# Optimization experiments

Hardware: AMD Instinct MI355X
Metric: run time of the kernel (lower is better)

Reference implementation:

```python
import jax, jax.numpy as jnp
import numpy as np
from math import ceil

EMBED = 512
HEADS = 8
HD = EMBED // HEADS  # 64
FFN = 2048
MIN_CHUNK = 32
LN_EPS = 1e-5


def layer_norm(x, g, b):
    mu = jnp.mean(x, axis=-1, keepdims=True)
    var = jnp.var(x, axis=-1, keepdims=True)
    return (x - mu) * jax.lax.rsqrt(var + LN_EPS) * g + b


def masked_attention(q, k, v, mask_bool, L):
    # q,k,v: [B*H, L, HD]; mask_bool: [B*H, L] (True = padding)
    BH = q.shape[0]
    S = max(MIN_CHUNK, ceil(L / 4))  # dynamic chunk size (static given L)
    C = ceil(L / S)
    pad = C * S - L
    if pad:
        q = jnp.pad(q, ((0, 0), (0, pad), (0, 0)))
        k = jnp.pad(k, ((0, 0), (0, pad), (0, 0)))
        v = jnp.pad(v, ((0, 0), (0, pad), (0, 0)))
        mask_bool = jnp.pad(mask_bool, ((0, 0), (0, pad)), constant_values=True)
    qc = q.reshape(BH, C, S, HD)
    kc = k.reshape(BH, C, S, HD)
    vc = v.reshape(BH, C, S, HD)
    mc = mask_bool.reshape(BH, C, S)
    # pad one phantom (fully masked) chunk on each side, then gather 3-chunk windows
    kp = jnp.pad(kc, ((0, 0), (1, 1), (0, 0), (0, 0)))
    vp = jnp.pad(vc, ((0, 0), (1, 1), (0, 0), (0, 0)))
    mp = jnp.pad(mc, ((0, 0), (1, 1), (0, 0)), constant_values=True)
    k_win = jnp.concatenate([kp[:, i:i + C] for i in range(3)], axis=2)  # [BH,C,3S,HD]
    v_win = jnp.concatenate([vp[:, i:i + C] for i in range(3)], axis=2)
    m_win = jnp.concatenate([mp[:, i:i + C] for i in range(3)], axis=2)  # [BH,C,3S]
    scores = jnp.einsum('bcqd,bckd->bcqk', qc, k_win) / jnp.sqrt(jnp.float32(HD))
    scores = jnp.where(m_win[:, :, None, :], -jnp.inf, scores)
    w = jax.nn.softmax(scores, axis=-1)
    out = jnp.einsum('bcqk,bckd->bcqd', w, v_win)
    return out.reshape(BH, C * S, HD)[:, :L]


def setup_inputs() -> dict:
    key = jax.random.key(0)
    ks = jax.random.split(key, 6)
    B, L, D = 4, 2048, EMBED
    s = 0.02
    return {
        'x': jax.random.normal(ks[0], (B, L, D), jnp.float32),
        'mask': jnp.zeros((B, L), jnp.int32),
        'qkv_w': jax.random.normal(ks[1], (D, 3 * D), jnp.float32) * s,
        'qkv_b': jnp.zeros((3 * D,), jnp.float32),
        'out_w': jax.random.normal(ks[2], (D, D), jnp.float32) * s,
        'out_b': jnp.zeros((D,), jnp.float32),
        'ffn_w1': jax.random.normal(ks[3], (D, FFN), jnp.float32) * s,
        'ffn_b1': jnp.zeros((FFN,), jnp.float32),
        'ffn_w2': jax.random.normal(ks[4], (FFN, D), jnp.float32) * s,
        'ffn_b2': jnp.zeros((D,), jnp.float32),
        'ln1_g': jnp.ones((D,), jnp.float32),
        'ln1_b': jnp.zeros((D,), jnp.float32),
        'ln2_g': jnp.ones((D,), jnp.float32),
        'ln2_b': jnp.zeros((D,), jnp.float32),
    }


def reference(x, mask, qkv_w, qkv_b, out_w, out_b, ffn_w1, ffn_b1, ffn_w2, ffn_b2, ln1_g, ln1_b, ln2_g, ln2_b):
    B, L, D = x.shape
    qkv = x @ qkv_w + qkv_b
    q, k, v = jnp.split(qkv, 3, axis=-1)

    def to_heads(t):
        return t.reshape(B, L, HEADS, HD).transpose(0, 2, 1, 3).reshape(B * HEADS, L, HD)

    mb = jnp.broadcast_to(mask.astype(bool)[:, None, :], (B, HEADS, L)).reshape(B * HEADS, L)
    a = masked_attention(to_heads(q), to_heads(k), to_heads(v), mb, L)
    a = a.reshape(B, HEADS, L, HD).transpose(0, 2, 1, 3).reshape(B, L, D)
    x = x + (a @ out_w + out_b)  # dropout is identity in eval
    x = layer_norm(x, ln1_g, ln1_b)
    h = jax.nn.gelu(x @ ffn_w1 + ffn_b1, approximate=False) @ ffn_w2 + ffn_b2
    x = layer_norm(x + h, ln2_g, ln2_b)
    return x
```

## Files before the change

### kernel.cpp

```cpp
#include <hip/hip_runtime.h>
#include <hip/hip_bf16.h>
#include <math.h>

#define EMBED 512
#define HEADS 8
#define HD    64
#define FFN_  2048
#define NB    4
#define LSEQ  2048
#define MROWS (NB*LSEQ)
#define BHN   (NB*HEADS)

typedef __attribute__((ext_vector_type(8))) short bf16x8;
typedef __attribute__((ext_vector_type(4))) float f32x4;
#define MFMA16(a,b,c) __builtin_amdgcn_mfma_f32_16x16x32_bf16(a,b,c,0,0,0)

__device__ __forceinline__ unsigned short f2bf(float f) {
    unsigned int u = __float_as_uint(f);
    u += 0x7fff + ((u >> 16) & 1);
    return (unsigned short)(u >> 16);
}
__device__ __forceinline__ float bf2f(unsigned short u) {
    return __uint_as_float(((unsigned int)u) << 16);
}
__device__ __forceinline__ unsigned int cvt_pk_bf16(float lo, float hi) {
    unsigned int r;
    asm("v_cvt_pk_bf16_f32 %0, %1, %2" : "=v"(r) : "v"(lo), "v"(hi));
    return r;
}
__device__ __forceinline__ void gl_lds16(const unsigned short* g, unsigned short* l) {
    __builtin_amdgcn_global_load_lds(
        (const __attribute__((address_space(1))) unsigned int*)g,
        (__attribute__((address_space(3))) unsigned int*)l, 16, 0, 0);
}
__device__ __forceinline__ float gelu_f(float x) {
    float u = x * fmaf(x * x, 0.044715f, 1.0f) * 0.7978845608f;
    float a = fminf(fmaxf(u * 2.885390082f, -30.f), 30.f);
    float t = __builtin_amdgcn_exp2f(a);
    return x * t * __builtin_amdgcn_rcpf(t + 1.0f);
}
__device__ __forceinline__ void xcd_swz(int& bx, int& by, int gx, int gy) {
    int nwg = gx * gy;
    int lid = by * gx + bx;
    int cpx = nwg >> 3;
    int swz = (lid & 7) * cpx + (lid >> 3);
    bx = swz % gx;
    by = swz / gx;
}


__global__ __launch_bounds__(256) void cvt_bf16(const float* __restrict__ in,
                                                unsigned short* __restrict__ out, int n) {
    int i = (blockIdx.x * 256 + threadIdx.x) * 8;
    if (i >= n) return;
    float4 a = *reinterpret_cast<const float4*>(&in[i]);
    float4 b = *reinterpret_cast<const float4*>(&in[i + 4]);
    unsigned short t[8] = {f2bf(a.x), f2bf(a.y), f2bf(a.z), f2bf(a.w),
                           f2bf(b.x), f2bf(b.y), f2bf(b.z), f2bf(b.w)};
    *reinterpret_cast<uint4*>(&out[i]) = *reinterpret_cast<uint4*>(t);
}

__global__ __launch_bounds__(256) void wtrans(const float* __restrict__ in,
                                              unsigned short* __restrict__ out,
                                              int K, int N) {
    __shared__ float tile[32][33];
    const int k0 = blockIdx.y * 32, n0 = blockIdx.x * 32;
    const int t = threadIdx.x;
    const int r = t >> 3, c = (t & 7) * 4;
    float4 v = *reinterpret_cast<const float4*>(&in[(size_t)(k0 + r) * N + n0 + c]);
    tile[r][c] = v.x; tile[r][c + 1] = v.y; tile[r][c + 2] = v.z; tile[r][c + 3] = v.w;
    __syncthreads();
    unsigned short tmp[4] = {f2bf(tile[c + 0][r]), f2bf(tile[c + 1][r]),
                             f2bf(tile[c + 2][r]), f2bf(tile[c + 3][r])};
    *reinterpret_cast<uint2*>(&out[(size_t)(n0 + r) * K + k0 + c]) =
        *reinterpret_cast<uint2*>(tmp);
}

__global__ __launch_bounds__(256) void vtransp(const unsigned short* __restrict__ v,
                                               unsigned short* __restrict__ vT) {
    __shared__ unsigned short tile[64][72];
    const int bh = blockIdx.y, l0 = blockIdx.x * 64;
    const int t = threadIdx.x;
    #pragma unroll
    for (int u = 0; u < 2; ++u) {
        int id = t + u * 256; int r = id >> 3, c = (id & 7) * 8;
        *reinterpret_cast<uint4*>(&tile[r][c]) = *reinterpret_cast<const uint4*>(
            &v[((size_t)bh * LSEQ + l0 + r) * HD + c]);
    }
    __syncthreads();
    #pragma unroll
    for (int u = 0; u < 2; ++u) {
        int id = t + u * 256; int d = id >> 3, kc = (id & 7) * 8;
        unsigned short tmp[8];
        #pragma unroll
        for (int jj = 0; jj < 8; ++jj) {
            int kap = kc + jj;
            tmp[jj] = tile[(kap & 3) * 16 + (kap >> 2)][d];
        }
        *reinterpret_cast<uint4*>(&vT[((size_t)bh * HD + d) * LSEQ + l0 + kc]) =
            *reinterpret_cast<uint4*>(tmp);
    }
}

template<int MODE>
__global__ __launch_bounds__(256) void gemm_bf16(
    const unsigned short* __restrict__ A, const unsigned short* __restrict__ WT,
    const float* __restrict__ bias,
    void* __restrict__ o0, void* __restrict__ o1, void* __restrict__ o2,
    int M, int N, int K)
{
    __shared__ unsigned short As[128 * 64];
    __shared__ unsigned short Bs[128 * 64];
    int bx = blockIdx.x, by = blockIdx.y;
    xcd_swz(bx, by, gridDim.x, gridDim.y);
    const int t = threadIdx.x;
    const int m0 = by * 128, n0 = bx * 128;
    const int w = t >> 6, lane = t & 63;
    const int wm = (w >> 1) * 64, wn = (w & 1) * 64;
    const int lr = lane & 15, lk = (lane >> 4) * 8;
    const int rb = (lane >> 4) * 4;
    const int srow = lane >> 3, scol = (lane & 7) * 8;

    f32x4 zero = {0.f, 0.f, 0.f, 0.f};
    f32x4 acc[4][4];
    #pragma unroll
    for (int i = 0; i < 4; ++i)
        #pragma unroll
        for (int j = 0; j < 4; ++j) acc[i][j] = zero;

    for (int k0 = 0; k0 < K; k0 += 64) {
        __syncthreads();
        #pragma unroll
        for (int i = 0; i < 4; ++i) {
            const int seg = w * 4 + i;
            const int r = seg * 8 + srow;
            gl_lds16(A  + (size_t)(m0 + r) * K + k0 + scol, &As[seg * 512 + lane * 8]);
            gl_lds16(WT + (size_t)(n0 + r) * K + k0 + scol, &Bs[seg * 512 + lane * 8]);
        }
        __syncthreads();
        #pragma unroll
        for (int kk = 0; kk < 2; ++kk) {
            bf16x8 a[4], b[4];
            #pragma unroll
            for (int i = 0; i < 4; ++i)
                a[i] = *reinterpret_cast<const bf16x8*>(&As[(wm + i * 16 + lr) * 64 + kk * 32 + lk]);
            #pragma unroll
            for (int j = 0; j < 4; ++j)
                b[j] = *reinterpret_cast<const bf16x8*>(&Bs[(wn + j * 16 + lr) * 64 + kk * 32 + lk]);
            #pragma unroll
            for (int i = 0; i < 4; ++i)
                #pragma unroll
                for (int j = 0; j < 4; ++j)
                    acc[i][j] = MFMA16(a[i], b[j], acc[i][j]);
        }
    }

    #pragma unroll
    for (int i = 0; i < 4; ++i) {
        #pragma unroll
        for (int j = 0; j < 4; ++j) {
            const int n = n0 + wn + j * 16 + lr;
            const float bv = bias[n];
            #pragma unroll
            for (int r = 0; r < 4; ++r) {
                const int m = m0 + wm + i * 16 + rb + r;
                float val = acc[i][j][r] + bv;
                if (MODE == 0) {
                    const int which = n >> 9, nn = n & 511, hs = nn >> 6, d = nn & 63;
                    const int bh = (m >> 11) * 8 + hs, l = m & 2047;
                    unsigned short* p = (which == 0) ? (unsigned short*)o0
                                      : (which == 1) ? (unsigned short*)o1
                                                     : (unsigned short*)o2;
                    p[((size_t)bh * LSEQ + l) * HD + d] = f2bf(val);
                } else {
                    size_t idx = (size_t)m * N + n;
                    ((unsigned short*)o0)[idx] = f2bf(gelu_f(val));
                }
            }
        }
    }
}

template<int MODE>
__global__ __launch_bounds__(256) void gemm64(
    const unsigned short* __restrict__ A, const unsigned short* __restrict__ WT,
    const float* __restrict__ bias, const void* __restrict__ res,
    void* __restrict__ out, int M, int N, int K)
{
    __shared__ unsigned short As[64 * 64];
    __shared__ unsigned short Bs[64 * 64];
    int bx = blockIdx.x, by = blockIdx.y;
    xcd_swz(bx, by, gridDim.x, gridDim.y);
    const int t = threadIdx.x;
    const int m0 = by * 64, n0 = bx * 64;
    const int w = t >> 6, lane = t & 63;
    const int wm = (w >> 1) * 32, wn = (w & 1) * 32;
    const int lr = lane & 15, lk = (lane >> 4) * 8;
    const int rb = (lane >> 4) * 4;
    const int srow = t >> 3, scol = (t & 7) * 8;

    f32x4 zero = {0.f, 0.f, 0.f, 0.f};
    f32x4 acc[2][2];
    #pragma unroll
    for (int i = 0; i < 2; ++i)
        #pragma unroll
        for (int j = 0; j < 2; ++j) acc[i][j] = zero;

    for (int k0 = 0; k0 < K; k0 += 64) {
        __syncthreads();
        gl_lds16(A  + (size_t)(m0 + srow)      * K + k0 + scol, &As[t * 8]);
        gl_lds16(A  + (size_t)(m0 + 32 + srow) * K + k0 + scol, &As[2048 + t * 8]);
        gl_lds16(WT + (size_t)(n0 + srow)      * K + k0 + scol, &Bs[t * 8]);
        gl_lds16(WT + (size_t)(n0 + 32 + srow) * K + k0 + scol, &Bs[2048 + t * 8]);
        __syncthreads();
        #pragma unroll
        for (int kk = 0; kk < 2; ++kk) {
            bf16x8 a[2], b[2];
            #pragma unroll
            for (int i = 0; i < 2; ++i)
                a[i] = *reinterpret_cast<const bf16x8*>(&As[(wm + i * 16 + lr) * 64 + kk * 32 + lk]);
            #pragma unroll
            for (int j = 0; j < 2; ++j)
                b[j] = *reinterpret_cast<const bf16x8*>(&Bs[(wn + j * 16 + lr) * 64 + kk * 32 + lk]);
            #pragma unroll
            for (int i = 0; i < 2; ++i)
                #pragma unroll
                for (int j = 0; j < 2; ++j)
                    acc[i][j] = MFMA16(a[i], b[j], acc[i][j]);
        }
    }

    #pragma unroll
    for (int i = 0; i < 2; ++i) {
        #pragma unroll
        for (int j = 0; j < 2; ++j) {
            const int n = n0 + wn + j * 16 + lr;
            const float bv = bias[n];
            #pragma unroll
            for (int r = 0; r < 4; ++r) {
                const int m = m0 + wm + i * 16 + rb + r;
                size_t idx = (size_t)m * N + n;
                float val = acc[i][j][r] + bv;
                if (MODE == 0) {
                    val += ((const float*)res)[idx];
                    ((unsigned short*)out)[idx] = f2bf(val);
                } else {
                    val += bf2f(((const unsigned short*)res)[idx]);
                    ((float*)out)[idx] = val;
                }
            }
        }
    }
}

__global__ __launch_bounds__(256) void attn_mfma(
    const unsigned short* __restrict__ Q, const unsigned short* __restrict__ K,
    const unsigned short* __restrict__ VTp, const int* __restrict__ mask,
    unsigned short* __restrict__ out)
{
    __shared__ unsigned short Ks[64][72];
    __shared__ unsigned short Vs[64][72];
    __shared__ unsigned short Ps[128][72];
    __shared__ float kbl[64];

    int bx = blockIdx.x, by = blockIdx.y;
    xcd_swz(bx, by, 16, 32);
    const int qt = bx, bh = by;
    const int b = bh >> 3, hh = bh & 7;
    const int t = threadIdx.x, w = t >> 6, lane = t & 63;
    const int lr = lane & 15, hi = lane >> 4;
    const int lk = hi * 8, rb = hi * 4;
    const int qr0 = qt * 128;
    const int c = qr0 >> 9;
    const int kstart = max(0, (c - 1) * 512), kend = min(LSEQ, (c + 2) * 512);

    const float C1  = 0.18033688f;
    const float KB0 = -14.4269504f;

    bf16x8 qf[2][2];
    #pragma unroll
    for (int fi = 0; fi < 2; ++fi)
        #pragma unroll
        for (int kk = 0; kk < 2; ++kk)
            qf[fi][kk] = *reinterpret_cast<const bf16x8*>(
                &Q[((size_t)bh * LSEQ + qr0 + w * 32 + fi * 16 + lr) * HD + kk * 32 + lk]);

    f32x4 zero = {0.f, 0.f, 0.f, 0.f};
    f32x4 acc[2][4];
    float lsum[2][4];
    #pragma unroll
    for (int fi = 0; fi < 2; ++fi) {
        #pragma unroll
        for (int j = 0; j < 4; ++j) acc[fi][j] = zero;
        #pragma unroll
        for (int r = 0; r < 4; ++r) lsum[fi][r] = 0.f;
    }

    for (int kg = kstart; kg < kend; kg += 64) {
        __syncthreads();
        #pragma unroll
        for (int u = 0; u < 2; ++u) {
            int id = t + u * 256; int r = id >> 3, kc = (id & 7) * 8;
            *reinterpret_cast<uint4*>(&Ks[r][kc]) = *reinterpret_cast<const uint4*>(
                &K[((size_t)bh * LSEQ + kg + r) * HD + kc]);
            *reinterpret_cast<uint4*>(&Vs[r][kc]) = *reinterpret_cast<const uint4*>(
                &VTp[((size_t)bh * HD + r) * LSEQ + kg + kc]);
        }
        if (t < 64) kbl[t] = mask[b * LSEQ + kg + t] ? -1e30f : KB0;
        __syncthreads();

        f32x4 s[2][4];
        #pragma unroll
        for (int fi = 0; fi < 2; ++fi)
            #pragma unroll
            for (int j = 0; j < 4; ++j) s[fi][j] = zero;
        #pragma unroll
        for (int kk = 0; kk < 2; ++kk) {
            #pragma unroll
            for (int j = 0; j < 4; ++j) {
                bf16x8 bk = *reinterpret_cast<const bf16x8*>(&Ks[j * 16 + lr][kk * 32 + lk]);
                s[0][j] = MFMA16(qf[0][kk], bk, s[0][j]);
                s[1][j] = MFMA16(qf[1][kk], bk, s[1][j]);
            }
        }
        #pragma unroll
        for (int fi = 0; fi < 2; ++fi) {
            #pragma unroll
            for (int r = 0; r < 4; ++r) {
                float p0 = __builtin_amdgcn_exp2f(fmaf(s[fi][0][r], C1, kbl[0 * 16 + lr]));
                float p1 = __builtin_amdgcn_exp2f(fmaf(s[fi][1][r], C1, kbl[1 * 16 + lr]));
                float p2 = __builtin_amdgcn_exp2f(fmaf(s[fi][2][r], C1, kbl[2 * 16 + lr]));
                float p3 = __builtin_amdgcn_exp2f(fmaf(s[fi][3][r], C1, kbl[3 * 16 + lr]));
                lsum[fi][r] += (p0 + p1) + (p2 + p3);
                uint2 pw;
                pw.x = cvt_pk_bf16(p0, p1);
                pw.y = cvt_pk_bf16(p2, p3);
                *reinterpret_cast<uint2*>(&Ps[w * 32 + fi * 16 + rb + r][lr * 4]) = pw;
            }
        }
        #pragma unroll
        for (int kk = 0; kk < 2; ++kk) {
            bf16x8 pa0 = *reinterpret_cast<const bf16x8*>(&Ps[w * 32 + lr][kk * 32 + lk]);
            bf16x8 pa1 = *reinterpret_cast<const bf16x8*>(&Ps[w * 32 + 16 + lr][kk * 32 + lk]);
            #pragma unroll
            for (int j = 0; j < 4; ++j) {
                bf16x8 bv = *reinterpret_cast<const bf16x8*>(&Vs[j * 16 + lr][kk * 32 + lk]);
                acc[0][j] = MFMA16(pa0, bv, acc[0][j]);
                acc[1][j] = MFMA16(pa1, bv, acc[1][j]);
            }
        }
    }

    float linv[2][4];
    #pragma unroll
    for (int fi = 0; fi < 2; ++fi)
        #pragma unroll
        for (int r = 0; r < 4; ++r) {
            float v = lsum[fi][r];
            v += __shfl_xor(v, 1, 16);
            v += __shfl_xor(v, 2, 16);
            v += __shfl_xor(v, 4, 16);
            v += __shfl_xor(v, 8, 16);
            linv[fi][r] = 1.0f / v;
        }
    #pragma unroll
    for (int fi = 0; fi < 2; ++fi)
        #pragma unroll
        for (int j = 0; j < 4; ++j)
            #pragma unroll
            for (int r = 0; r < 4; ++r) {
                const int l = qr0 + w * 32 + fi * 16 + rb + r;
                const int d = j * 16 + lr;
                out[((size_t)(b * LSEQ + l)) * EMBED + hh * HD + d] =
                    f2bf(acc[fi][j][r] * linv[fi][r]);
            }
}

__global__ __launch_bounds__(256) void ln_b2b(
    const unsigned short* __restrict__ in, const float* __restrict__ g,
    const float* __restrict__ bt, unsigned short* __restrict__ out)
{
    const int t = threadIdx.x, lane = t & 63;
    const int row = blockIdx.x * 4 + (t >> 6);
    uint4 raw = *reinterpret_cast<const uint4*>(&in[(size_t)row * EMBED + lane * 8]);
    float v[8];
    const unsigned int* rw = reinterpret_cast<const unsigned int*>(&raw);
    #pragma unroll
    for (int i = 0; i < 4; ++i) {
        v[2 * i]     = __uint_as_float(rw[i] << 16);
        v[2 * i + 1] = __uint_as_float(rw[i] & 0xffff0000u);
    }
    float s = 0.f, ss = 0.f;
    #pragma unroll
    for (int i = 0; i < 8; ++i) { s += v[i]; ss += v[i] * v[i]; }
    #pragma unroll
    for (int off = 1; off < 64; off <<= 1) {
        s  += __shfl_xor(s, off);
        ss += __shfl_xor(ss, off);
    }
    const float mu = s * (1.0f / EMBED);
    const float var = ss * (1.0f / EMBED) - mu * mu;
    const float rs = rsqrtf(var + 1e-5f);
    float4 g0 = *reinterpret_cast<const float4*>(&g[lane * 8]);
    float4 g1 = *reinterpret_cast<const float4*>(&g[lane * 8 + 4]);
    float4 b0 = *reinterpret_cast<const float4*>(&bt[lane * 8]);
    float4 b1 = *reinterpret_cast<const float4*>(&bt[lane * 8 + 4]);
    float gg[8] = {g0.x, g0.y, g0.z, g0.w, g1.x, g1.y, g1.z, g1.w};
    float bb[8] = {b0.x, b0.y, b0.z, b0.w, b1.x, b1.y, b1.z, b1.w};
    unsigned short o[8];
    #pragma unroll
    for (int i = 0; i < 8; ++i) o[i] = f2bf((v[i] - mu) * rs * gg[i] + bb[i]);
    *reinterpret_cast<uint4*>(&out[(size_t)row * EMBED + lane * 8]) =
        *reinterpret_cast<uint4*>(o);
}

__global__ __launch_bounds__(256) void ln_f2f(
    const float* __restrict__ in, const float* __restrict__ g,
    const float* __restrict__ bt, float* __restrict__ out)
{
    const int t = threadIdx.x, lane = t & 63;
    const int row = blockIdx.x * 4 + (t >> 6);
    const float* x = in + (size_t)row * EMBED + lane * 8;
    float4 a = *reinterpret_cast<const float4*>(x);
    float4 b2 = *reinterpret_cast<const float4*>(x + 4);
    float v[8] = {a.x, a.y, a.z, a.w, b2.x, b2.y, b2.z, b2.w};
    float s = 0.f, ss = 0.f;
    #pragma unroll
    for (int i = 0; i < 8; ++i) { s += v[i]; ss += v[i] * v[i]; }
    #pragma unroll
    for (int off = 1; off < 64; off <<= 1) {
        s  += __shfl_xor(s, off);
        ss += __shfl_xor(ss, off);
    }
    const float mu = s * (1.0f / EMBED);
    const float var = ss * (1.0f / EMBED) - mu * mu;
    const float rs = rsqrtf(var + 1e-5f);
    float4 g0 = *reinterpret_cast<const float4*>(&g[lane * 8]);
    float4 g1 = *reinterpret_cast<const float4*>(&g[lane * 8 + 4]);
    float4 b0 = *reinterpret_cast<const float4*>(&bt[lane * 8]);
    float4 b1 = *reinterpret_cast<const float4*>(&bt[lane * 8 + 4]);
    float gg[8] = {g0.x, g0.y, g0.z, g0.w, g1.x, g1.y, g1.z, g1.w};
    float bb[8] = {b0.x, b0.y, b0.z, b0.w, b1.x, b1.y, b1.z, b1.w};
    float o[8];
    #pragma unroll
    for (int i = 0; i < 8; ++i) o[i] = (v[i] - mu) * rs * gg[i] + bb[i];
    float* op = out + (size_t)row * EMBED + lane * 8;
    *reinterpret_cast<float4*>(op)     = make_float4(o[0], o[1], o[2], o[3]);
    *reinterpret_cast<float4*>(op + 4) = make_float4(o[4], o[5], o[6], o[7]);
}

extern "C" void kernel_launch(void* const* d_in, const int* in_sizes, int n_in,
                              void* d_out, int out_size, void* d_ws, size_t ws_size,
                              hipStream_t stream) {
    const float* x      = (const float*)d_in[0];
    const int*   mask   = (const int*)  d_in[1];
    const float* qkv_w  = (const float*)d_in[2];
    const float* qkv_b  = (const float*)d_in[3];
    const float* out_w  = (const float*)d_in[4];
    const float* out_b  = (const float*)d_in[5];
    const float* ffn_w1 = (const float*)d_in[6];
    const float* ffn_b1 = (const float*)d_in[7];
    const float* ffn_w2 = (const float*)d_in[8];
    const float* ffn_b2 = (const float*)d_in[9];
    const float* ln1_g  = (const float*)d_in[10];
    const float* ln1_b  = (const float*)d_in[11];
    const float* ln2_g  = (const float*)d_in[12];
    const float* ln2_b  = (const float*)d_in[13];

    char* wsb = (char*)d_ws;
    unsigned short* qkv_wT = (unsigned short*)(wsb + 0);
    unsigned short* out_wT = (unsigned short*)(wsb + 1572864);
    unsigned short* w1T    = (unsigned short*)(wsb + 2097152);
    unsigned short* w2T    = (unsigned short*)(wsb + 4194304);
    unsigned short* xb     = (unsigned short*)(wsb + 6291456);
    unsigned short* qb     = (unsigned short*)(wsb + 14680064);
    unsigned short* kbuf   = (unsigned short*)(wsb + 23068672);
    unsigned short* vb     = (unsigned short*)(wsb + 31457280);
    unsigned short* y      = (unsigned short*)(wsb + 39845888);
    unsigned short* vTp    = xb;
    unsigned short* am     = vb;
    unsigned short* xlnb   = xb;
    unsigned short* h      = (unsigned short*)(wsb + 31457280);
    float*          z      = (float*)(wsb + 65011712);

    cvt_bf16<<<MROWS * EMBED / 8 / 256, 256, 0, stream>>>(x, xb, MROWS * EMBED);
    wtrans<<<dim3(1536 / 32, 512 / 32),  256, 0, stream>>>(qkv_w,  qkv_wT, 512, 1536);
    wtrans<<<dim3(512 / 32,  512 / 32),  256, 0, stream>>>(out_w,  out_wT, 512, 512);
    wtrans<<<dim3(2048 / 32, 512 / 32),  256, 0, stream>>>(ffn_w1, w1T,    512, 2048);
    wtrans<<<dim3(512 / 32,  2048 / 32), 256, 0, stream>>>(ffn_w2, w2T,    2048, 512);

    gemm_bf16<0><<<dim3(1536 / 128, MROWS / 128), 256, 0, stream>>>(
        xb, qkv_wT, qkv_b, qb, kbuf, vb, MROWS, 1536, 512);
    vtransp<<<dim3(LSEQ / 64, BHN), 256, 0, stream>>>(vb, vTp);
    attn_mfma<<<dim3(LSEQ / 128, BHN), 256, 0, stream>>>(qb, kbuf, vTp, mask, am);
    gemm64<0><<<dim3(EMBED / 64, MROWS / 64), 256, 0, stream>>>(
        am, out_wT, out_b, x, y, MROWS, EMBED, 512);
    ln_b2b<<<MROWS / 4, 256, 0, stream>>>(y, ln1_g, ln1_b, xlnb);
    gemm_bf16<2><<<dim3(FFN_ / 128, MROWS / 128), 256, 0, stream>>>(
        xlnb, w1T, ffn_b1, h, nullptr, nullptr, MROWS, FFN_, 512);
    gemm64<1><<<dim3(EMBED / 64, MROWS / 64), 256, 0, stream>>>(
        h, w2T, ffn_b2, xlnb, z, MROWS, EMBED, FFN_);
    ln_f2f<<<MROWS / 4, 256, 0, stream>>>(z, ln2_g, ln2_b, (float*)d_out);
}
```

Measured before the change: 286.1 us.

## Double-buffer GEMM LDS tiles and split attention across 8 waves

Both GEMM kernels now keep two LDS tile buffers, issuing the next K-tile's global-to-LDS loads before computing the current one. They use explicit vmcnt waits and raw barriers so load latency overlaps MFMA work. The attention kernel goes from 256 to 512 threads, each wave handling 16 query rows instead of 32, for more waves in flight and fewer registers per thread. The costs are doubled LDS in the GEMMs, which may lower occupancy, and halved MFMA reuse of each K/V fragment per wave in attention.

Result: faster. 276.1 us (-3.5%).

```diff
diff --git a/kernel.cpp b/kernel.cpp
--- a/kernel.cpp
+++ b/kernel.cpp
@@ -109,8 +109,8 @@
     void* __restrict__ o0, void* __restrict__ o1, void* __restrict__ o2,
     int M, int N, int K)
 {
-    __shared__ unsigned short As[128 * 64];
-    __shared__ unsigned short Bs[128 * 64];
+    __shared__ unsigned short As[2][128 * 64];
+    __shared__ unsigned short Bs[2][128 * 64];
     int bx = blockIdx.x, by = blockIdx.y;
     xcd_swz(bx, by, gridDim.x, gridDim.y);
     const int t = threadIdx.x;
@@ -128,31 +128,44 @@
         #pragma unroll
         for (int j = 0; j < 4; ++j) acc[i][j] = zero;
 
-    for (int k0 = 0; k0 < K; k0 += 64) {
-        __syncthreads();
+    auto stage = [&](int buf, int k0) {
         #pragma unroll
         for (int i = 0; i < 4; ++i) {
             const int seg = w * 4 + i;
             const int r = seg * 8 + srow;
-            gl_lds16(A  + (size_t)(m0 + r) * K + k0 + scol, &As[seg * 512 + lane * 8]);
-            gl_lds16(WT + (size_t)(n0 + r) * K + k0 + scol, &Bs[seg * 512 + lane * 8]);
-        }
-        __syncthreads();
+            gl_lds16(A  + (size_t)(m0 + r) * K + k0 + scol, &As[buf][seg * 512 + lane * 8]);
+            gl_lds16(WT + (size_t)(n0 + r) * K + k0 + scol, &Bs[buf][seg * 512 + lane * 8]);
+        }
+    };
+
+    const int nk = K >> 6;
+    stage(0, 0);
+    for (int ti = 0; ti < nk; ++ti) {
+        if (ti + 1 < nk) {
+            stage((ti + 1) & 1, (ti + 1) << 6);
+            asm volatile("s_waitcnt vmcnt(8)" ::: "memory");
+        } else {
+            asm volatile("s_waitcnt vmcnt(0)" ::: "memory");
+        }
+        __builtin_amdgcn_s_barrier();
+        const unsigned short* as = As[ti & 1];
+        const unsigned short* bs = Bs[ti & 1];
         #pragma unroll
         for (int kk = 0; kk < 2; ++kk) {
             bf16x8 a[4], b[4];
             #pragma unroll
             for (int i = 0; i < 4; ++i)
-                a[i] = *reinterpret_cast<const bf16x8*>(&As[(wm + i * 16 + lr) * 64 + kk * 32 + lk]);
+                a[i] = *reinterpret_cast<const bf16x8*>(&as[(wm + i * 16 + lr) * 64 + kk * 32 + lk]);
             #pragma unroll
             for (int j = 0; j < 4; ++j)
-                b[j] = *reinterpret_cast<const bf16x8*>(&Bs[(wn + j * 16 + lr) * 64 + kk * 32 + lk]);
+                b[j] = *reinterpret_cast<const bf16x8*>(&bs[(wn + j * 16 + lr) * 64 + kk * 32 + lk]);
             #pragma unroll
             for (int i = 0; i < 4; ++i)
                 #pragma unroll
                 for (int j = 0; j < 4; ++j)
                     acc[i][j] = MFMA16(a[i], b[j], acc[i][j]);
         }
+        __builtin_amdgcn_s_barrier();
     }
 
     #pragma unroll
@@ -187,8 +200,8 @@
     const float* __restrict__ bias, const void* __restrict__ res,
     void* __restrict__ out, int M, int N, int K)
 {
-    __shared__ unsigned short As[64 * 64];
-    __shared__ unsigned short Bs[64 * 64];
+    __shared__ unsigned short As[2][64 * 64];
+    __shared__ unsigned short Bs[2][64 * 64];
     int bx = blockIdx.x, by = blockIdx.y;
     xcd_swz(bx, by, gridDim.x, gridDim.y);
     const int t = threadIdx.x;
@@ -206,28 +219,41 @@
         #pragma unroll
         for (int j = 0; j < 2; ++j) acc[i][j] = zero;
 
-    for (int k0 = 0; k0 < K; k0 += 64) {
-        __syncthreads();
-        gl_lds16(A  + (size_t)(m0 + srow)      * K + k0 + scol, &As[t * 8]);
-        gl_lds16(A  + (size_t)(m0 + 32 + srow) * K + k0 + scol, &As[2048 + t * 8]);
-        gl_lds16(WT + (size_t)(n0 + srow)      * K + k0 + scol, &Bs[t * 8]);
-        gl_lds16(WT + (size_t)(n0 + 32 + srow) * K + k0 + scol, &Bs[2048 + t * 8]);
-        __syncthreads();
+    auto stage = [&](int buf, int k0) {
+        gl_lds16(A  + (size_t)(m0 + srow)      * K + k0 + scol, &As[buf][t * 8]);
+        gl_lds16(A  + (size_t)(m0 + 32 + srow) * K + k0 + scol, &As[buf][2048 + t * 8]);
+        gl_lds16(WT + (size_t)(n0 + srow)      * K + k0 + scol, &Bs[buf][t * 8]);
+        gl_lds16(WT + (size_t)(n0 + 32 + srow) * K + k0 + scol, &Bs[buf][2048 + t * 8]);
+    };
+
+    const int nk = K >> 6;
+    stage(0, 0);
+    for (int ti = 0; ti < nk; ++ti) {
+        if (ti + 1 < nk) {
+            stage((ti + 1) & 1, (ti + 1) << 6);
+            asm volatile("s_waitcnt vmcnt(4)" ::: "memory");
+        } else {
+            asm volatile("s_waitcnt vmcnt(0)" ::: "memory");
+        }
+        __builtin_amdgcn_s_barrier();
+        const unsigned short* as = As[ti & 1];
+        const unsigned short* bs = Bs[ti & 1];
         #pragma unroll
         for (int kk = 0; kk < 2; ++kk) {
             bf16x8 a[2], b[2];
             #pragma unroll
             for (int i = 0; i < 2; ++i)
-                a[i] = *reinterpret_cast<const bf16x8*>(&As[(wm + i * 16 + lr) * 64 + kk * 32 + lk]);
+                a[i] = *reinterpret_cast<const bf16x8*>(&as[(wm + i * 16 + lr) * 64 + kk * 32 + lk]);
             #pragma unroll
             for (int j = 0; j < 2; ++j)
-                b[j] = *reinterpret_cast<const bf16x8*>(&Bs[(wn + j * 16 + lr) * 64 + kk * 32 + lk]);
+                b[j] = *reinterpret_cast<const bf16x8*>(&bs[(wn + j * 16 + lr) * 64 + kk * 32 + lk]);
             #pragma unroll
             for (int i = 0; i < 2; ++i)
                 #pragma unroll
                 for (int j = 0; j < 2; ++j)
                     acc[i][j] = MFMA16(a[i], b[j], acc[i][j]);
         }
+        __builtin_amdgcn_s_barrier();
     }
 
     #pragma unroll
@@ -253,7 +279,7 @@
     }
 }
 
-__global__ __launch_bounds__(256) void attn_mfma(
+__global__ __launch_bounds__(512) void attn_mfma(
     const unsigned short* __restrict__ Q, const unsigned short* __restrict__ K,
     const unsigned short* __restrict__ VTp, const int* __restrict__ mask,
     unsigned short* __restrict__ out)
@@ -277,103 +303,83 @@
     const float C1  = 0.18033688f;
     const float KB0 = -14.4269504f;
 
-    bf16x8 qf[2][2];
-    #pragma unroll
-    for (int fi = 0; fi < 2; ++fi)
-        #pragma unroll
-        for (int kk = 0; kk < 2; ++kk)
-            qf[fi][kk] = *reinterpret_cast<const bf16x8*>(
-                &Q[((size_t)bh * LSEQ + qr0 + w * 32 + fi * 16 + lr) * HD + kk * 32 + lk]);
+    bf16x8 qf[2];
+    #pragma unroll
+    for (int kk = 0; kk < 2; ++kk)
+        qf[kk] = *reinterpret_cast<const bf16x8*>(
+            &Q[((size_t)bh * LSEQ + qr0 + w * 16 + lr) * HD + kk * 32 + lk]);
 
     f32x4 zero = {0.f, 0.f, 0.f, 0.f};
-    f32x4 acc[2][4];
-    float lsum[2][4];
-    #pragma unroll
-    for (int fi = 0; fi < 2; ++fi) {
-        #pragma unroll
-        for (int j = 0; j < 4; ++j) acc[fi][j] = zero;
-        #pragma unroll
-        for (int r = 0; r < 4; ++r) lsum[fi][r] = 0.f;
-    }
+    f32x4 acc[4];
+    float lsum[4] = {0.f, 0.f, 0.f, 0.f};
+    #pragma unroll
+    for (int j = 0; j < 4; ++j) acc[j] = zero;
 
     for (int kg = kstart; kg < kend; kg += 64) {
         __syncthreads();
-        #pragma unroll
-        for (int u = 0; u < 2; ++u) {
-            int id = t + u * 256; int r = id >> 3, kc = (id & 7) * 8;
+        {
+            int r = t >> 3, kc = (t & 7) * 8;
             *reinterpret_cast<uint4*>(&Ks[r][kc]) = *reinterpret_cast<const uint4*>(
                 &K[((size_t)bh * LSEQ + kg + r) * HD + kc]);
             *reinterpret_cast<uint4*>(&Vs[r][kc]) = *reinterpret_cast<const uint4*>(
                 &VTp[((size_t)bh * HD + r) * LSEQ + kg + kc]);
-        }
-        if (t < 64) kbl[t] = mask[b * LSEQ + kg + t] ? -1e30f : KB0;
+            if (t < 64) kbl[t] = mask[b * LSEQ + kg + t] ? -1e30f : KB0;
+        }
         __syncthreads();
 
-        f32x4 s[2][4];
-        #pragma unroll
-        for (int fi = 0; fi < 2; ++fi)
-            #pragma unroll
-            for (int j = 0; j < 4; ++j) s[fi][j] = zero;
+        f32x4 s[4];
+        #pragma unroll
+        for (int j = 0; j < 4; ++j) s[j] = zero;
         #pragma unroll
         for (int kk = 0; kk < 2; ++kk) {
             #pragma unroll
             for (int j = 0; j < 4; ++j) {
                 bf16x8 bk = *reinterpret_cast<const bf16x8*>(&Ks[j * 16 + lr][kk * 32 + lk]);
-                s[0][j] = MFMA16(qf[0][kk], bk, s[0][j]);
-                s[1][j] = MFMA16(qf[1][kk], bk, s[1][j]);
+                s[j] = MFMA16(qf[kk], bk, s[j]);
             }
         }
         #pragma unroll
-        for (int fi = 0; fi < 2; ++fi) {
-            #pragma unroll
-            for (int r = 0; r < 4; ++r) {
-                float p0 = __builtin_amdgcn_exp2f(fmaf(s[fi][0][r], C1, kbl[0 * 16 + lr]));
-                float p1 = __builtin_amdgcn_exp2f(fmaf(s[fi][1][r], C1, kbl[1 * 16 + lr]));
-                float p2 = __builtin_amdgcn_exp2f(fmaf(s[fi][2][r], C1, kbl[2 * 16 + lr]));
-                float p3 = __builtin_amdgcn_exp2f(fmaf(s[fi][3][r], C1, kbl[3 * 16 + lr]));
-                lsum[fi][r] += (p0 + p1) + (p2 + p3);
-                uint2 pw;
-                pw.x = cvt_pk_bf16(p0, p1);
-                pw.y = cvt_pk_bf16(p2, p3);
-                *reinterpret_cast<uint2*>(&Ps[w * 32 + fi * 16 + rb + r][lr * 4]) = pw;
-            }
+        for (int r = 0; r < 4; ++r) {
+            float p0 = __builtin_amdgcn_exp2f(fmaf(s[0][r], C1, kbl[0 * 16 + lr]));
+            float p1 = __builtin_amdgcn_exp2f(fmaf(s[1][r], C1, kbl[1 * 16 + lr]));
+            float p2 = __builtin_amdgcn_exp2f(fmaf(s[2][r], C1, kbl[2 * 16 + lr]));
+            float p3 = __builtin_amdgcn_exp2f(fmaf(s[3][r], C1, kbl[3 * 16 + lr]));
+            lsum[r] += (p0 + p1) + (p2 + p3);
+            uint2 pw;
+            pw.x = cvt_pk_bf16(p0, p1);
+            pw.y = cvt_pk_bf16(p2, p3);
+            *reinterpret_cast<uint2*>(&Ps[w * 16 + rb + r][lr * 4]) = pw;
         }
         #pragma unroll
         for (int kk = 0; kk < 2; ++kk) {
-            bf16x8 pa0 = *reinterpret_cast<const bf16x8*>(&Ps[w * 32 + lr][kk * 32 + lk]);
-            bf16x8 pa1 = *reinterpret_cast<const bf16x8*>(&Ps[w * 32 + 16 + lr][kk * 32 + lk]);
+            bf16x8 pa = *reinterpret_cast<const bf16x8*>(&Ps[w * 16 + lr][kk * 32 + lk]);
             #pragma unroll
             for (int j = 0; j < 4; ++j) {
                 bf16x8 bv = *reinterpret_cast<const bf16x8*>(&Vs[j * 16 + lr][kk * 32 + lk]);
-                acc[0][j] = MFMA16(pa0, bv, acc[0][j]);
-                acc[1][j] = MFMA16(pa1, bv, acc[1][j]);
+                acc[j] = MFMA16(pa, bv, acc[j]);
             }
         }
     }
 
-    float linv[2][4];
-    #pragma unroll
-    for (int fi = 0; fi < 2; ++fi)
+    float linv[4];
+    #pragma unroll
+    for (int r = 0; r < 4; ++r) {
+        float v = lsum[r];
+        v += __shfl_xor(v, 1, 16);
+        v += __shfl_xor(v, 2, 16);
+        v += __shfl_xor(v, 4, 16);
+        v += __shfl_xor(v, 8, 16);
+        linv[r] = 1.0f / v;
+    }
+    #pragma unroll
+    for (int j = 0; j < 4; ++j)
         #pragma unroll
         for (int r = 0; r < 4; ++r) {
-            float v = lsum[fi][r];
-            v += __shfl_xor(v, 1, 16);
-            v += __shfl_xor(v, 2, 16);
-            v += __shfl_xor(v, 4, 16);
-            v += __shfl_xor(v, 8, 16);
-            linv[fi][r] = 1.0f / v;
-        }
-    #pragma unroll
-    for (int fi = 0; fi < 2; ++fi)
-        #pragma unroll
-        for (int j = 0; j < 4; ++j)
-            #pragma unroll
-            for (int r = 0; r < 4; ++r) {
-                const int l = qr0 + w * 32 + fi * 16 + rb + r;
-                const int d = j * 16 + lr;
-                out[((size_t)(b * LSEQ + l)) * EMBED + hh * HD + d] =
-                    f2bf(acc[fi][j][r] * linv[fi][r]);
-            }
+            const int l = qr0 + w * 16 + rb + r;
+            const int d = j * 16 + lr;
+            out[((size_t)(b * LSEQ + l)) * EMBED + hh * HD + d] =
+                f2bf(acc[j][r] * linv[r]);
+        }
 }
 
 __global__ __launch_bounds__(256) void ln_b2b(
@@ -492,7 +498,7 @@
     gemm_bf16<0><<<dim3(1536 / 128, MROWS / 128), 256, 0, stream>>>(
         xb, qkv_wT, qkv_b, qb, kbuf, vb, MROWS, 1536, 512);
     vtransp<<<dim3(LSEQ / 64, BHN), 256, 0, stream>>>(vb, vTp);
-    attn_mfma<<<dim3(LSEQ / 128, BHN), 256, 0, stream>>>(qb, kbuf, vTp, mask, am);
+    attn_mfma<<<dim3(LSEQ / 128, BHN), 512, 0, stream>>>(qb, kbuf, vTp, mask, am);
     gemm64<0><<<dim3(EMBED / 64, MROWS / 64), 256, 0, stream>>>(
         am, out_wT, out_b, x, y, MROWS, EMBED, 512);
     ln_b2b<<<MROWS / 4, 256, 0, stream>>>(y, ln1_g, ln1_b, xlnb);
```
